# Optimization experiments

Hardware: AMD Instinct MI355X
Metric: run time of the kernel (lower is better)

The kernel has to match this reference:

```python
import jax, jax.numpy as jnp
import numpy as np

B, T, V, E, H, C = 128, 512, 100000, 100, 128, 3


def _lstm_dir(xs, w_ih, w_hh, b, reverse=False):
    # xs: [T,B,D]; w_ih: [4H,D]; w_hh: [4H,H]; b: [4H] (b_ih+b_hh combined)
    Tn, Bn, _ = xs.shape
    Hn = w_hh.shape[1]
    if reverse:
        xs = xs[::-1]
    gx = jnp.einsum('tbd,gd->tbg', xs, w_ih) + b  # [T,B,4H] input projections

    def step(carry, g_in):
        h, c = carry
        gates = g_in + h @ w_hh.T
        i, f, g, o = jnp.split(gates, 4, axis=-1)  # torch gate order i,f,g,o
        i = jax.nn.sigmoid(i)
        f = jax.nn.sigmoid(f)
        g = jnp.tanh(g)
        o = jax.nn.sigmoid(o)
        c = f * c + i * g
        h = o * jnp.tanh(c)
        return (h, c), h

    init = (jnp.zeros((Bn, Hn), xs.dtype), jnp.zeros((Bn, Hn), xs.dtype))
    (h_last, _), hs = jax.lax.scan(step, init, gx)
    if reverse:
        hs = hs[::-1]
    return hs, h_last


def setup_inputs() -> dict:
    key = jax.random.key(0)
    ks = jax.random.split(key, 24)
    s_e = 1.0 / np.sqrt(H)

    def u(k, shape):
        return jax.random.uniform(k, shape, jnp.float32, -s_e, s_e)

    x = jax.random.randint(ks[0], (B, T), 0, V, dtype=jnp.int32)
    emb = jax.random.normal(ks[1], (V, E), jnp.float32)
    emb = emb.at[0].set(0.0)  # padding_idx=0
    inp = {'x': x, 'emb': emb}
    names = []
    idx = 2
    for layer, din in ((0, E), (1, 2 * H)):
        for suf in ('', 'r'):
            inp[f'w_ih_l{layer}{suf}'] = u(ks[idx], (4 * H, din)); idx += 1
            inp[f'w_hh_l{layer}{suf}'] = u(ks[idx], (4 * H, H)); idx += 1
            inp[f'b_ih_l{layer}{suf}'] = u(ks[idx], (4 * H,)); idx += 1
            inp[f'b_hh_l{layer}{suf}'] = u(ks[idx], (4 * H,)); idx += 1
    s_f = 1.0 / np.sqrt(2 * H)
    inp['fc_w'] = jax.random.uniform(ks[22], (C, 2 * H), jnp.float32, -s_f, s_f)
    inp['fc_b'] = jax.random.uniform(ks[23], (C,), jnp.float32, -s_f, s_f)
    return inp


def reference(x, emb, w_ih_l0, w_hh_l0, b_ih_l0, b_hh_l0,
              w_ih_l0r, w_hh_l0r, b_ih_l0r, b_hh_l0r,
              w_ih_l1, w_hh_l1, b_ih_l1, b_hh_l1,
              w_ih_l1r, w_hh_l1r, b_ih_l1r, b_hh_l1r,
              fc_w, fc_b):
    # dropout is identity in eval mode
    xe = emb[x]                      # [B,T,E]
    xs = jnp.transpose(xe, (1, 0, 2))  # [T,B,E]
    # layer 0 bidirectional
    hf0, _ = _lstm_dir(xs, w_ih_l0, w_hh_l0, b_ih_l0 + b_hh_l0, reverse=False)
    hb0, _ = _lstm_dir(xs, w_ih_l0r, w_hh_l0r, b_ih_l0r + b_hh_l0r, reverse=True)
    x1 = jnp.concatenate([hf0, hb0], axis=-1)  # [T,B,2H]
    # layer 1 bidirectional; only final hidden states needed
    _, hF = _lstm_dir(x1, w_ih_l1, w_hh_l1, b_ih_l1 + b_hh_l1, reverse=False)
    _, hB = _lstm_dir(x1, w_ih_l1r, w_hh_l1r, b_ih_l1r + b_hh_l1r, reverse=True)
    out = jnp.concatenate([hF, hB], axis=1)  # [B,2H] == cat(hidden[-2], hidden[-1])
    return out @ fc_w.T + fc_b  # [B,C]
```

## Files before the change

kernel.cpp:

```cpp
#include <hip/hip_runtime.h>
#include <hip/hip_bf16.h>
#include <math.h>

#define TT 512
#define BB 128
#define EE 100
#define HH 128
#define G4 512
#define K1 256

typedef __attribute__((ext_vector_type(8))) short bf16x8;
typedef __attribute__((ext_vector_type(4))) float f32x4;

__device__ inline unsigned short bf16_rne(float v) {
    __hip_bfloat16 h = __float2bfloat16(v);
    return *reinterpret_cast<unsigned short*>(&h);
}

__device__ inline void gload16(const void* g, void* l) {
    __builtin_amdgcn_global_load_lds(
        (const __attribute__((address_space(1))) void*)g,
        (__attribute__((address_space(3))) void*)l, 16, 0, 0);
}

template<int CTRL>
__device__ inline float dppf(float x) {
    int r = __builtin_amdgcn_update_dpp(0, __float_as_int(x), CTRL, 0xF, 0xF, true);
    return __int_as_float(r);
}
template<int CTRL>
__device__ inline float4 dpp4f(float4 v) {
    float4 r;
    r.x = dppf<CTRL>(v.x); r.y = dppf<CTRL>(v.y);
    r.z = dppf<CTRL>(v.z); r.w = dppf<CTRL>(v.w);
    return r;
}

__global__ void embed_cvt(const int* __restrict__ x, const float* __restrict__ emb,
                          unsigned short* __restrict__ xs2) {
    int row = blockIdx.x;
    int k = threadIdx.x;
    int b = row & 127, t = row >> 7;
    int tok = x[b * TT + t];
    float v = (k < EE) ? emb[(size_t)tok * EE + k] : 0.f;
    xs2[(size_t)row * 128 + k] = bf16_rne(v);
}

__global__ void wcvt2(const float* __restrict__ srcf, const float* __restrict__ srcr,
                      int Kin, int Kp,
                      unsigned short* __restrict__ dstf, unsigned short* __restrict__ dstr) {
    const float* src = blockIdx.y ? srcr : srcf;
    unsigned short* dst = blockIdx.y ? dstr : dstf;
    int n = blockIdx.x;
    int k = threadIdx.x;
    int j = n & 3;
    int gate = ((j & 1) << 1) | (j >> 1);
    int r = gate * 128 + (n >> 2);
    float v = (k < Kin) ? src[(size_t)r * Kin + k] : 0.f;
    dst[(size_t)n * Kp + k] = bf16_rne(v);
}

__global__ void bias2(const float* __restrict__ bihf0, const float* __restrict__ bhhf0,
                      const float* __restrict__ bihr0, const float* __restrict__ bhhr0,
                      const float* __restrict__ bihf1, const float* __restrict__ bhhf1,
                      const float* __restrict__ bihr1, const float* __restrict__ bhhr1,
                      float* __restrict__ dst) {
    int n = blockIdx.x * 256 + threadIdx.x;
    int layer = n >> 10;
    int d = (n >> 9) & 1, m = n & 511;
    int j = m & 3;
    int gate = ((j & 1) << 1) | (j >> 1);
    int src = gate * 128 + (m >> 2);
    const float* a = layer ? (d ? bihr1 : bihf1) : (d ? bihr0 : bihf0);
    const float* c = layer ? (d ? bhhr1 : bhhf1) : (d ? bhhr0 : bhhf0);
    dst[n] = a[src] + c[src];
}

__global__ void whh_pack4(const float* __restrict__ w0f, const float* __restrict__ w0r,
                          const float* __restrict__ w1f, const float* __restrict__ w1r,
                          float* __restrict__ dstbase) {
    int which = blockIdx.y;
    const float* src = which == 0 ? w0f : which == 1 ? w0r : which == 2 ? w1f : w1r;
    float* dst = dstbase + (size_t)which * 128 * 128 * 4;
    int u = blockIdx.x;
    int t = threadIdx.x;
    int q = t >> 5, m = (t >> 3) & 3, kk = t & 7;
    int k = 32 * q + 8 * ((u & 3) ^ m) + kk;
    float4 v;
    v.x = src[((size_t)(0 * 128 + u)) * 128 + k];
    v.y = src[((size_t)(1 * 128 + u)) * 128 + k];
    v.z = src[((size_t)(2 * 128 + u)) * 128 + k];
    v.w = src[((size_t)(3 * 128 + u)) * 128 + k];
    reinterpret_cast<float4*>(dst)[(size_t)u * 128 + t] = v;
}

template<int K2>
__global__ __launch_bounds__(256) void gemm_mfma(
    const unsigned short* __restrict__ A2,
    const unsigned short* __restrict__ W2cat,
    const float* __restrict__ biascat,
    float* __restrict__ Cf, float* __restrict__ Cr,
    int t_base)
{
    __shared__ bf16x8 As[1024];
    __shared__ bf16x8 Bs[1024];
    int tid = threadIdx.x;
    int s = blockIdx.y;
    int dir = blockIdx.x >> 2;
    int nBase = (blockIdx.x & 3) * 128;
    int t = dir ? (TT - 1 - t_base - s) : (t_base + s);
    float* C = dir ? Cr : Cf;
    const unsigned short* Abase = A2 + (size_t)t * BB * K2;
    const unsigned short* Wbase = W2cat + (size_t)(dir * 512 + nBase) * K2;
    int lane = tid & 63, wid = tid >> 6;
    int wr = wid >> 1, wc = wid & 1;
    int l15 = lane & 15, g = lane >> 4;

    f32x4 acc[4][4];
    const f32x4 z = {0.f, 0.f, 0.f, 0.f};
    #pragma unroll
    for (int i = 0; i < 4; ++i)
        #pragma unroll
        for (int j = 0; j < 4; ++j) acc[i][j] = z;

    for (int kt = 0; kt < K2 / 64; ++kt) {
        #pragma unroll
        for (int j = 0; j < 4; ++j) {
            int p = tid + j * 256;
            int row = p >> 3;
            int k16 = (p & 7) ^ (row & 7);
            size_t goff = (size_t)row * K2 + kt * 64 + k16 * 8;
            gload16(Abase + goff, &As[p]);
            gload16(Wbase + goff, &Bs[p]);
        }
        __syncthreads();
        #pragma unroll
        for (int ks = 0; ks < 2; ++ks) {
            bf16x8 af[4], bfr[4];
            #pragma unroll
            for (int i = 0; i < 4; ++i) {
                int arow = wr * 64 + i * 16 + l15;
                int abyte = arow * 128 + ((ks * 64 + g * 16) ^ ((arow & 7) << 4));
                af[i] = As[abyte >> 4];
                int brow = wc * 64 + i * 16 + l15;
                int bbyte = brow * 128 + ((ks * 64 + g * 16) ^ ((brow & 7) << 4));
                bfr[i] = Bs[bbyte >> 4];
            }
            #pragma unroll
            for (int i = 0; i < 4; ++i)
                #pragma unroll
                for (int j = 0; j < 4; ++j)
                    acc[i][j] = __builtin_amdgcn_mfma_f32_16x16x32_bf16(
                        af[i], bfr[j], acc[i][j], 0, 0, 0);
        }
        __syncthreads();
    }
    #pragma unroll
    for (int i = 0; i < 4; ++i) {
        size_t crow0 = (size_t)s * 128 + wr * 64 + i * 16 + g * 4;
        #pragma unroll
        for (int j = 0; j < 4; ++j) {
            int col = nBase + wc * 64 + j * 16 + l15;
            float bsum = biascat[dir * 512 + col];
            #pragma unroll
            for (int r = 0; r < 4; ++r)
                C[(crow0 + r) * G4 + col] = acc[i][j][r] + bsum;
        }
    }
}

__device__ inline float sig_fast(float z) {
    return __builtin_amdgcn_rcpf(1.f + __expf(-z));
}

__global__ __launch_bounds__(512, 2) void lstm_chunk(
    const float* __restrict__ gxf,
    const float* __restrict__ gxr,
    const float* __restrict__ wpkf,
    const float* __restrict__ wpkr,
    float* __restrict__ h_state,
    float* __restrict__ c_state,
    unsigned short* __restrict__ out_x1,
    int t_base, int TC, int init)
{
    int blk = blockIdx.x;
    int dir = blk >> 7;
    int b   = blk & 127;
    const float* gx  = dir ? gxr : gxf;
    const float* wpk = dir ? wpkr : wpkf;
    int tid = threadIdx.x;
    int u = tid >> 2, q = tid & 3, jj = u & 3;

    const f32x4* wp4 = reinterpret_cast<const f32x4*>(wpk) + ((size_t)u * 128 + q * 32);
#define LW(i) const f32x4 w##i = wp4[i];
    LW(0)  LW(1)  LW(2)  LW(3)  LW(4)  LW(5)  LW(6)  LW(7)
    LW(8)  LW(9)  LW(10) LW(11) LW(12) LW(13) LW(14) LW(15)
    LW(16) LW(17) LW(18) LW(19) LW(20) LW(21) LW(22) LW(23)
    LW(24) LW(25) LW(26) LW(27) LW(28) LW(29) LW(30) LW(31)
#undef LW

    __shared__ float hb[2][144];
    int sbase = (dir * BB + b) * HH;
    int hslot = (u >> 5) * 36 + (u & 31);
    float c = init ? 0.f : c_state[sbase + u];
    float h = init ? 0.f : h_state[sbase + u];
    if (q == 0) hb[0][hslot] = h;
    __syncthreads();

    int roff = 36 * q + 8 * jj;
    const float* gxrow = gx + b * G4 + tid;
    float gin = gxrow[0];
    bool odd2 = (q & 2) != 0;
    float fq = (q == 1) ? 2.f : 1.f;
    float bq = (q == 1) ? -1.f : 0.f;

    for (int s = 0; s < TC; ++s) {
        int p = s & 1;
        int sn = (s + 1 < TC) ? s + 1 : s;
        float gin_next = gxrow[(size_t)sn * BB * G4];

        const float4* hp = reinterpret_cast<const float4*>(&hb[p][roff]);
        float4 hA = hp[0], hB = hp[1];
        float4 c1A = dpp4f<0x1B>(dpp4f<0x141>(hA));
        float4 c1B = dpp4f<0x1B>(dpp4f<0x141>(hB));
        float4 c2A = dpp4f<0x128>(hA);
        float4 c2B = dpp4f<0x128>(hB);
        float4 c3A = dpp4f<0x128>(c1A);
        float4 c3B = dpp4f<0x128>(c1B);

        f32x4 a0 = {0.f,0.f,0.f,0.f}, a1 = {0.f,0.f,0.f,0.f};
        f32x4 a2 = {0.f,0.f,0.f,0.f}, a3 = {0.f,0.f,0.f,0.f};
#define FMA1(W, HV, A) A = __builtin_elementwise_fma(W, f32x4{HV, HV, HV, HV}, A)
        FMA1(w0,  hA.x, a0);  FMA1(w1,  hA.y, a1);  FMA1(w2,  hA.z, a2);  FMA1(w3,  hA.w, a3);
        FMA1(w4,  hB.x, a0);  FMA1(w5,  hB.y, a1);  FMA1(w6,  hB.z, a2);  FMA1(w7,  hB.w, a3);
        FMA1(w8,  c1A.x, a0); FMA1(w9,  c1A.y, a1); FMA1(w10, c1A.z, a2); FMA1(w11, c1A.w, a3);
        FMA1(w12, c1B.x, a0); FMA1(w13, c1B.y, a1); FMA1(w14, c1B.z, a2); FMA1(w15, c1B.w, a3);
        FMA1(w16, c2A.x, a0); FMA1(w17, c2A.y, a1); FMA1(w18, c2A.z, a2); FMA1(w19, c2A.w, a3);
        FMA1(w20, c2B.x, a0); FMA1(w21, c2B.y, a1); FMA1(w22, c2B.z, a2); FMA1(w23, c2B.w, a3);
        FMA1(w24, c3A.x, a0); FMA1(w25, c3A.y, a1); FMA1(w26, c3A.z, a2); FMA1(w27, c3A.w, a3);
        FMA1(w28, c3B.x, a0); FMA1(w29, c3B.y, a1); FMA1(w30, c3B.z, a2); FMA1(w31, c3B.w, a3);
#undef FMA1
        f32x4 acc = (a0 + a1) + (a2 + a3);

        float xs = acc.x + dppf<0xB1>(acc.x);
        float ys = acc.y + dppf<0xB1>(acc.y);
        float zs = acc.z + dppf<0xB1>(acc.z);
        float ws = acc.w + dppf<0xB1>(acc.w);
        bool oddq = (q & 1) != 0;
        float sa = oddq ? zs : xs;
        float sb = oddq ? ws : ys;
        float sa2 = sa + dppf<0x4E>(sa);
        float sb2 = sb + dppf<0x4E>(sb);
        float pre_dot = odd2 ? sb2 : sa2;

        float pre = pre_dot + gin;
        float act = __builtin_fmaf(sig_fast(pre * fq), fq, bq);

        float ig = dppf<0x00>(act);
        float gg = dppf<0x55>(act);
        float fg = dppf<0xAA>(act);
        float og = dppf<0xFF>(act);

        c = fg * c + ig * gg;
        float th = __builtin_fmaf(2.f, sig_fast(2.f * c), -1.f);
        h = og * th;

        if (q == 0) {
            hb[p ^ 1][hslot] = h;
            if (out_x1) {
                int tg = dir ? (TT - 1 - (t_base + s)) : (t_base + s);
                out_x1[((size_t)tg * BB + b) * 256 + dir * HH + u] = bf16_rne(h);
            }
        }
        asm volatile("s_waitcnt lgkmcnt(0)" ::: "memory");
        __builtin_amdgcn_s_barrier();
        asm volatile("" ::: "memory");
        gin = gin_next;
    }
    if (q == 0) {
        h_state[sbase + u] = h;
        c_state[sbase + u] = c;
    }
}

__global__ void fc_kernel(const float* __restrict__ h_state,
                          const float* __restrict__ fc_w,
                          const float* __restrict__ fc_b,
                          float* __restrict__ out) {
    int tid = blockIdx.x * blockDim.x + threadIdx.x;
    if (tid >= BB * 3) return;
    int b = tid / 3;
    int c = tid % 3;
    float acc = 0.f;
    for (int j = 0; j < 256; ++j) {
        float v = (j < HH) ? h_state[((size_t)0 * BB + b) * HH + j]
                           : h_state[((size_t)1 * BB + b) * HH + (j - HH)];
        acc += v * fc_w[c * 256 + j];
    }
    out[b * 3 + c] = acc + fc_b[c];
}

extern "C" void kernel_launch(void* const* d_in, const int* in_sizes, int n_in,
                              void* d_out, int out_size, void* d_ws, size_t ws_size,
                              hipStream_t stream) {
    const int*   x        = (const int*)  d_in[0];
    const float* emb      = (const float*)d_in[1];
    const float* w_ih_l0  = (const float*)d_in[2];
    const float* w_hh_l0  = (const float*)d_in[3];
    const float* b_ih_l0  = (const float*)d_in[4];
    const float* b_hh_l0  = (const float*)d_in[5];
    const float* w_ih_l0r = (const float*)d_in[6];
    const float* w_hh_l0r = (const float*)d_in[7];
    const float* b_ih_l0r = (const float*)d_in[8];
    const float* b_hh_l0r = (const float*)d_in[9];
    const float* w_ih_l1  = (const float*)d_in[10];
    const float* w_hh_l1  = (const float*)d_in[11];
    const float* b_ih_l1  = (const float*)d_in[12];
    const float* b_hh_l1  = (const float*)d_in[13];
    const float* w_ih_l1r = (const float*)d_in[14];
    const float* w_hh_l1r = (const float*)d_in[15];
    const float* b_ih_l1r = (const float*)d_in[16];
    const float* b_hh_l1r = (const float*)d_in[17];
    const float* fc_w     = (const float*)d_in[18];
    const float* fc_b     = (const float*)d_in[19];
    float* out = (float*)d_out;
    (void)in_sizes; (void)n_in; (void)out_size;

    size_t xs2_b   = (size_t)TT * BB * 128 * 2;
    size_t x1_b    = (size_t)TT * BB * 256 * 2;
    size_t w2l0_b  = (size_t)512 * 128 * 2;
    size_t w2l1_b  = (size_t)512 * 256 * 2;
    size_t bias_b  = (size_t)1024 * 4;
    size_t wpk_b   = (size_t)128 * 128 * 4 * 4;
    size_t state_b = (size_t)2 * BB * HH * 4;
    size_t fixed = xs2_b + x1_b + 2 * w2l0_b + 2 * w2l1_b + 2 * bias_b
                 + 4 * wpk_b + 2 * state_b + 4096;
    int TC = 512;
    while (TC > 8) {
        size_t chunk2 = (size_t)TC * BB * G4 * 4 * 2;
        if (fixed + chunk2 <= ws_size) break;
        TC >>= 1;
    }
    char* ws = (char*)d_ws;
    size_t off = 0;
    unsigned short* xs2   = (unsigned short*)(ws + off); off += xs2_b;
    unsigned short* x1_2  = (unsigned short*)(ws + off); off += x1_b;
    unsigned short* w2l0f = (unsigned short*)(ws + off); off += w2l0_b;
    unsigned short* w2l0r = (unsigned short*)(ws + off); off += w2l0_b;
    unsigned short* w2l1f = (unsigned short*)(ws + off); off += w2l1_b;
    unsigned short* w2l1r = (unsigned short*)(ws + off); off += w2l1_b;
    float* biasl0  = (float*)(ws + off); off += bias_b;
    float* biasl1  = (float*)(ws + off); off += bias_b;
    float* wpk0f   = (float*)(ws + off); off += wpk_b;
    float* wpk0r   = (float*)(ws + off); off += wpk_b;
    float* wpk1f   = (float*)(ws + off); off += wpk_b;
    float* wpk1r   = (float*)(ws + off); off += wpk_b;
    float* h_state = (float*)(ws + off); off += state_b;
    float* c_state = (float*)(ws + off); off += state_b;
    float* gxf     = (float*)(ws + off); off += (size_t)TC * BB * G4 * 4;
    float* gxr     = (float*)(ws + off);
    (void)biasl1;

    int NC = TT / TC;
    dim3 ggrid(8, TC);

    embed_cvt<<<TT * BB, 128, 0, stream>>>(x, emb, xs2);
    wcvt2<<<dim3(512, 2), 128, 0, stream>>>(w_ih_l0, w_ih_l0r, EE, 128, w2l0f, w2l0r);
    wcvt2<<<dim3(512, 2), 256, 0, stream>>>(w_ih_l1, w_ih_l1r, K1, 256, w2l1f, w2l1r);
    bias2<<<8, 256, 0, stream>>>(b_ih_l0, b_hh_l0, b_ih_l0r, b_hh_l0r,
                                 b_ih_l1, b_hh_l1, b_ih_l1r, b_hh_l1r, biasl0);
    whh_pack4<<<dim3(128, 4), 128, 0, stream>>>(w_hh_l0, w_hh_l0r, w_hh_l1, w_hh_l1r, wpk0f);

    for (int ci = 0; ci < NC; ++ci) {
        int t0 = ci * TC;
        gemm_mfma<128><<<ggrid, 256, 0, stream>>>(xs2, w2l0f, biasl0, gxf, gxr, t0);
        lstm_chunk<<<256, 512, 0, stream>>>(gxf, gxr, wpk0f, wpk0r,
                                            h_state, c_state, x1_2, t0, TC, ci == 0);
    }
    for (int ci = 0; ci < NC; ++ci) {
        int t0 = ci * TC;
        gemm_mfma<256><<<ggrid, 256, 0, stream>>>(x1_2, w2l1f, biasl1, gxf, gxr, t0);
        lstm_chunk<<<256, 512, 0, stream>>>(gxf, gxr, wpk1f, wpk1r,
                                            h_state, c_state, nullptr, t0, TC, ci == 0);
    }
    fc_kernel<<<2, 192, 0, stream>>>(h_state, fc_w, fc_b, out);
}
```

Measured before the change: 887.4 us.

## Read h from LDS directly and vectorize gate-projection GEMM epilogue stores

```diff
diff --git a/kernel.cpp b/kernel.cpp
--- a/kernel.cpp
+++ b/kernel.cpp
@@ -27,13 +27,6 @@
 __device__ inline float dppf(float x) {
     int r = __builtin_amdgcn_update_dpp(0, __float_as_int(x), CTRL, 0xF, 0xF, true);
     return __int_as_float(r);
-}
-template<int CTRL>
-__device__ inline float4 dpp4f(float4 v) {
-    float4 r;
-    r.x = dppf<CTRL>(v.x); r.y = dppf<CTRL>(v.y);
-    r.z = dppf<CTRL>(v.z); r.w = dppf<CTRL>(v.w);
-    return r;
 }
 
 __global__ void embed_cvt(const int* __restrict__ x, const float* __restrict__ emb,
@@ -83,15 +76,13 @@
     const float* src = which == 0 ? w0f : which == 1 ? w0r : which == 2 ? w1f : w1r;
     float* dst = dstbase + (size_t)which * 128 * 128 * 4;
     int u = blockIdx.x;
-    int t = threadIdx.x;
-    int q = t >> 5, m = (t >> 3) & 3, kk = t & 7;
-    int k = 32 * q + 8 * ((u & 3) ^ m) + kk;
+    int k = threadIdx.x;
     float4 v;
     v.x = src[((size_t)(0 * 128 + u)) * 128 + k];
     v.y = src[((size_t)(1 * 128 + u)) * 128 + k];
     v.z = src[((size_t)(2 * 128 + u)) * 128 + k];
     v.w = src[((size_t)(3 * 128 + u)) * 128 + k];
-    reinterpret_cast<float4*>(dst)[(size_t)u * 128 + t] = v;
+    reinterpret_cast<float4*>(dst)[(size_t)u * 128 + k] = v;
 }
 
 template<int K2>
@@ -155,16 +146,37 @@
         }
         __syncthreads();
     }
+    int l3 = l15 & 3;
+    int cquad = l15 & 12;
+    bool lb0 = (l15 & 1) != 0;
+    bool lb1 = (l15 & 2) != 0;
     #pragma unroll
     for (int i = 0; i < 4; ++i) {
-        size_t crow0 = (size_t)s * 128 + wr * 64 + i * 16 + g * 4;
+        int row = s * 128 + wr * 64 + i * 16 + g * 4 + l3;
+        float* Crow = C + (size_t)row * G4;
         #pragma unroll
         for (int j = 0; j < 4; ++j) {
-            int col = nBase + wc * 64 + j * 16 + l15;
-            float bsum = biascat[dir * 512 + col];
-            #pragma unroll
-            for (int r = 0; r < 4; ++r)
-                C[(crow0 + r) * G4 + col] = acc[i][j][r] + bsum;
+            int colb = nBase + wc * 64 + j * 16 + cquad;
+            float4 bv = *reinterpret_cast<const float4*>(&biascat[dir * 512 + colb]);
+            f32x4 v = acc[i][j];
+            float t0 = dppf<0xB1>(v[1]);
+            float t1 = dppf<0xB1>(v[0]);
+            float t2 = dppf<0xB1>(v[3]);
+            float t3 = dppf<0xB1>(v[2]);
+            float T0 = lb0 ? t0 : v[0];
+            float T1 = lb0 ? v[1] : t1;
+            float T2 = lb0 ? t2 : v[2];
+            float T3 = lb0 ? v[3] : t3;
+            float s0 = dppf<0x4E>(T2);
+            float s1 = dppf<0x4E>(T3);
+            float s2 = dppf<0x4E>(T0);
+            float s3 = dppf<0x4E>(T1);
+            float W0 = lb1 ? s0 : T0;
+            float W1 = lb1 ? s1 : T1;
+            float W2 = lb1 ? T2 : s2;
+            float W3 = lb1 ? T3 : s3;
+            float4 outv = {W0 + bv.x, W1 + bv.y, W2 + bv.z, W3 + bv.w};
+            *reinterpret_cast<float4*>(&Crow[colb]) = outv;
         }
     }
 }
@@ -189,7 +201,7 @@
     const float* gx  = dir ? gxr : gxf;
     const float* wpk = dir ? wpkr : wpkf;
     int tid = threadIdx.x;
-    int u = tid >> 2, q = tid & 3, jj = u & 3;
+    int u = tid >> 2, q = tid & 3;
 
     const f32x4* wp4 = reinterpret_cast<const f32x4*>(wpk) + ((size_t)u * 128 + q * 32);
 #define LW(i) const f32x4 w##i = wp4[i];
@@ -199,15 +211,14 @@
     LW(24) LW(25) LW(26) LW(27) LW(28) LW(29) LW(30) LW(31)
 #undef LW
 
-    __shared__ float hb[2][144];
+    __shared__ float hb[2][160];
     int sbase = (dir * BB + b) * HH;
-    int hslot = (u >> 5) * 36 + (u & 31);
+    int hslot = (u >> 5) * 40 + (u & 31);
     float c = init ? 0.f : c_state[sbase + u];
     float h = init ? 0.f : h_state[sbase + u];
     if (q == 0) hb[0][hslot] = h;
     __syncthreads();
 
-    int roff = 36 * q + 8 * jj;
     const float* gxrow = gx + b * G4 + tid;
     float gin = gxrow[0];
     bool odd2 = (q & 2) != 0;
@@ -219,27 +230,21 @@
         int sn = (s + 1 < TC) ? s + 1 : s;
         float gin_next = gxrow[(size_t)sn * BB * G4];
 
-        const float4* hp = reinterpret_cast<const float4*>(&hb[p][roff]);
-        float4 hA = hp[0], hB = hp[1];
-        float4 c1A = dpp4f<0x1B>(dpp4f<0x141>(hA));
-        float4 c1B = dpp4f<0x1B>(dpp4f<0x141>(hB));
-        float4 c2A = dpp4f<0x128>(hA);
-        float4 c2B = dpp4f<0x128>(hB);
-        float4 c3A = dpp4f<0x128>(c1A);
-        float4 c3B = dpp4f<0x128>(c1B);
+        const float4* hb4 = reinterpret_cast<const float4*>(&hb[p][40 * q]);
+        float4 hv0 = hb4[0], hv1 = hb4[1], hv2 = hb4[2], hv3 = hb4[3];
+        float4 hv4 = hb4[4], hv5 = hb4[5], hv6 = hb4[6], hv7 = hb4[7];
 
         f32x4 a0 = {0.f,0.f,0.f,0.f}, a1 = {0.f,0.f,0.f,0.f};
         f32x4 a2 = {0.f,0.f,0.f,0.f}, a3 = {0.f,0.f,0.f,0.f};
-#define FMA1(W, HV, A) A = __builtin_elementwise_fma(W, f32x4{HV, HV, HV, HV}, A)
-        FMA1(w0,  hA.x, a0);  FMA1(w1,  hA.y, a1);  FMA1(w2,  hA.z, a2);  FMA1(w3,  hA.w, a3);
-        FMA1(w4,  hB.x, a0);  FMA1(w5,  hB.y, a1);  FMA1(w6,  hB.z, a2);  FMA1(w7,  hB.w, a3);
-        FMA1(w8,  c1A.x, a0); FMA1(w9,  c1A.y, a1); FMA1(w10, c1A.z, a2); FMA1(w11, c1A.w, a3);
-        FMA1(w12, c1B.x, a0); FMA1(w13, c1B.y, a1); FMA1(w14, c1B.z, a2); FMA1(w15, c1B.w, a3);
-        FMA1(w16, c2A.x, a0); FMA1(w17, c2A.y, a1); FMA1(w18, c2A.z, a2); FMA1(w19, c2A.w, a3);
-        FMA1(w20, c2B.x, a0); FMA1(w21, c2B.y, a1); FMA1(w22, c2B.z, a2); FMA1(w23, c2B.w, a3);
-        FMA1(w24, c3A.x, a0); FMA1(w25, c3A.y, a1); FMA1(w26, c3A.z, a2); FMA1(w27, c3A.w, a3);
-        FMA1(w28, c3B.x, a0); FMA1(w29, c3B.y, a1); FMA1(w30, c3B.z, a2); FMA1(w31, c3B.w, a3);
-#undef FMA1
+#define FM(i0,i1,i2,i3,HV) { \
+        f32x4 hh; \
+        hh = f32x4{HV.x,HV.x,HV.x,HV.x}; a0 = __builtin_elementwise_fma(w##i0, hh, a0); \
+        hh = f32x4{HV.y,HV.y,HV.y,HV.y}; a1 = __builtin_elementwise_fma(w##i1, hh, a1); \
+        hh = f32x4{HV.z,HV.z,HV.z,HV.z}; a2 = __builtin_elementwise_fma(w##i2, hh, a2); \
+        hh = f32x4{HV.w,HV.w,HV.w,HV.w}; a3 = __builtin_elementwise_fma(w##i3, hh, a3); }
+        FM(0,1,2,3,hv0)    FM(4,5,6,7,hv1)    FM(8,9,10,11,hv2)  FM(12,13,14,15,hv3)
+        FM(16,17,18,19,hv4) FM(20,21,22,23,hv5) FM(24,25,26,27,hv6) FM(28,29,30,31,hv7)
+#undef FM
         f32x4 acc = (a0 + a1) + (a2 + a3);
 
         float xs = acc.x + dppf<0xB1>(acc.x);
@@ -359,7 +364,6 @@
     float* c_state = (float*)(ws + off); off += state_b;
     float* gxf     = (float*)(ws + off); off += (size_t)TC * BB * G4 * 4;
     float* gxr     = (float*)(ws + off);
-    (void)biasl1;
 
     int NC = TT / TC;
     dim3 ggrid(8, TC);
```

After: 824.0 us. 1.08x faster.
